# Performance work log

Measured on AMD Instinct MI355X. Metric: run time of the kernel, lower is better.

## Reference

```python
import jax, jax.numpy as jnp
import numpy as np

B, TIN, E, TOUT, NMEL = 32, 512, 576, 400, 80
PRE, ARNN, DRNN, ADIM, NF, KS = 256, 1024, 1024, 128, 32, 31


def setup_inputs() -> dict:
    key = jax.random.key(0)
    ks = jax.random.split(key, 24)
    r = lambda i, sh, s=0.02: jax.random.normal(ks[i], sh, dtype=jnp.float32) * s
    return {
        'memory': jax.random.normal(ks[0], (B, TIN, E), dtype=jnp.float32) * 0.5,
        'decoder_inputs': jax.random.normal(ks[1], (B, TOUT, NMEL), dtype=jnp.float32) * 0.5,
        'prenet_W1': r(2, (PRE, NMEL)),
        'prenet_W2': r(3, (PRE, PRE)),
        'att_Wih': r(4, (4 * ARNN, PRE + E)),
        'att_Whh': r(5, (4 * ARNN, ARNN)),
        'att_bih': r(6, (4 * ARNN,)),
        'att_bhh': r(7, (4 * ARNN,)),
        'qW': r(8, (ADIM, ARNN)),
        'memW': r(9, (ADIM, E)),
        'convW': r(10, (NF, 2, KS)),
        'convb': r(11, (NF,)),
        'locW': r(12, (ADIM, NF)),
        'vW': r(13, (ADIM,)),
        'dec_Wih': r(14, (4 * DRNN, ARNN + E)),
        'dec_Whh': r(15, (4 * DRNN, DRNN)),
        'dec_bih': r(16, (4 * DRNN,)),
        'dec_bhh': r(17, (4 * DRNN,)),
        'projW': r(18, (NMEL, DRNN + E)),
        'projb': r(19, (NMEL,)),
        'gateW': r(20, (1, DRNN + E)),
        'gateb': r(21, (1,)),
        'memory_lengths': jnp.clip(jax.random.randint(ks[22], (B,), 1, TIN + 1), 16, TIN),
    }


def _lstm(x, h, c, Wih, Whh, bih, bhh):
    g = x @ Wih.T + bih + h @ Whh.T + bhh
    i, f, gg, o = jnp.split(g, 4, axis=-1)  # torch LSTMCell gate order i,f,g,o
    c = jax.nn.sigmoid(f) * c + jax.nn.sigmoid(i) * jnp.tanh(gg)
    h = jax.nn.sigmoid(o) * jnp.tanh(c)
    return h, c


def _forward(memory, decoder_inputs, prenet_W1, prenet_W2, att_Wih, att_Whh, att_bih,
             att_bhh, qW, memW, convW, convb, locW, vW, dec_Wih, dec_Whh, dec_bih,
             dec_bhh, projW, projb, gateW, gateb, memory_lengths):
    b, tin, e = memory.shape
    # go frame + teacher forcing inputs -> prenet (dropout off in deterministic eval)
    go = jnp.zeros((b, 1, NMEL), dtype=memory.dtype)
    di = jnp.concatenate([go, decoder_inputs], axis=1)          # [B, T+1, NMEL]
    x = jax.nn.relu(di @ prenet_W1.T)
    x = jax.nn.relu(x @ prenet_W2.T)                            # [B, T+1, PRE]
    xs = jnp.swapaxes(x, 0, 1)[:-1]                             # [T, B, PRE]
    pmem = memory @ memW.T                                      # [B, TIN, ADIM]
    invalid = jnp.arange(tin)[None, :] >= memory_lengths[:, None]
    pad = KS // 2

    init = (jnp.zeros((b, ARNN)), jnp.zeros((b, ARNN)),
            jnp.zeros((b, DRNN)), jnp.zeros((b, DRNN)),
            jnp.zeros((b, tin)), jnp.zeros((b, tin)),
            jnp.zeros((b, e)))

    def step(carry, xt):
        ah, ac, dh, dc, aw, awc, ctx = carry
        ci = jnp.concatenate([xt, ctx], axis=-1)
        ah, ac = _lstm(ci, ah, ac, att_Wih, att_Whh, att_bih, att_bhh)
        ah = ac  # faithful to source: dropout(attention_cell) overwrites hidden (identity in eval)
        wc = jnp.stack([aw, awc], axis=1)                       # [B, 2, TIN]
        loc = jax.lax.conv_general_dilated(
            wc, convW, (1,), [(pad, pad)],
            dimension_numbers=('NCH', 'OIH', 'NCH')) + convb[None, :, None]
        loc = jnp.swapaxes(loc, 1, 2) @ locW.T                  # [B, TIN, ADIM]
        q = (ah @ qW.T)[:, None, :]                             # [B, 1, ADIM]
        en = jnp.tanh(q + pmem + loc) @ vW                      # [B, TIN]
        en = jnp.where(invalid, -jnp.inf, en)
        aw = jax.nn.softmax(en, axis=1)
        ctx = jnp.einsum('bt,bte->be', aw, memory)
        awc = awc + aw
        d_in = jnp.concatenate([ah, ctx], axis=-1)
        dh, dc = _lstm(d_in, dh, dc, dec_Wih, dec_Whh, dec_bih, dec_bhh)
        dhc = jnp.concatenate([dh, ctx], axis=-1)
        mel = dhc @ projW.T + projb                             # [B, NMEL]
        gate = (dhc @ gateW.T + gateb)[:, 0]                    # [B]
        return (ah, ac, dh, dc, aw, awc, ctx), (mel, gate, aw)

    _, (mels, gates, aligns) = jax.lax.scan(step, init, xs)
    mel_out = jnp.swapaxes(jnp.swapaxes(mels, 0, 1), 1, 2)      # [B, NMEL, T]
    gate_out = jnp.swapaxes(gates, 0, 1)                        # [B, T]
    align_out = jnp.swapaxes(aligns, 0, 1)                      # [B, T, TIN]
    return mel_out, gate_out, align_out


def reference(memory, decoder_inputs, prenet_W1, prenet_W2, att_Wih, att_Whh, att_bih,
              att_bhh, qW, memW, convW, convb, locW, vW, dec_Wih, dec_Whh, dec_bih,
              dec_bhh, projW, projb, gateW, gateb, memory_lengths):
    return _forward(memory, decoder_inputs, prenet_W1, prenet_W2, att_Wih, att_Whh,
                    att_bih, att_bhh, qW, memW, convW, convb, locW, vW, dec_Wih,
                    dec_Whh, dec_bih, dec_bhh, projW, projb, gateW, gateb,
                    memory_lengths)
```

## Files before the change

### kernel.cpp

```cpp
#include <hip/hip_runtime.h>
#include <stdint.h>


#define NB  32
#define TI  512
#define ED  576
#define TO  400
#define NM  80
#define PR  256
#define AR  1024
#define DR  1024
#define AD  128
#define NFl 32
#define KSz 31
#define KA  1856
#define KD  2624
#define NKT_A 58
#define NKT_D 82
#define REL_IDX 320
#define MF_OFF  512

#define SCR_CWB 3584
#define SCR_ACC 4608
#define SCR_DCC 4736
#define SCR_SQ  4864
#define LDS_WA_BYTES (NKT_A*512*2)
#define LDS_WD_BYTES (NKT_D*512*2)
#define LDS_SCR_FLOATS 4992
#define LDS_TOTAL (LDS_WA_BYTES + LDS_WD_BYTES + LDS_SCR_FLOATS*4)

typedef __attribute__((ext_vector_type(8))) short bf8_t;
typedef __attribute__((ext_vector_type(4))) float f4_t;
typedef __attribute__((ext_vector_type(2))) float f2_t;
typedef unsigned long long ull;

__device__ __forceinline__ short f2bf(float f){
  union { float f; unsigned u; } v; v.f = f;
  unsigned r = v.u + 0x7fffu + ((v.u >> 16) & 1u);
  return (short)(r >> 16);
}
__device__ __forceinline__ float bf2f(short s){
  union { unsigned u; float f; } v; v.u = ((unsigned)(unsigned short)s) << 16; return v.f;
}
__device__ __forceinline__ float sigm(float x){ return 1.f / (1.f + __expf(-x)); }

__device__ __forceinline__ f4_t MFMA(bf8_t a, bf8_t b, f4_t c){
  return __builtin_amdgcn_mfma_f32_16x16x32_bf16(a, b, c, 0, 0, 0);
}

__device__ __forceinline__ float cld(const float* p){
  return __hip_atomic_load(p, __ATOMIC_RELAXED, __HIP_MEMORY_SCOPE_AGENT);
}
__device__ __forceinline__ void cst(float* p, float v){
  __hip_atomic_store(p, v, __ATOMIC_RELAXED, __HIP_MEMORY_SCOPE_AGENT);
}
__device__ __forceinline__ ull cld8(const void* p){
  return __hip_atomic_load((const ull*)p, __ATOMIC_RELAXED, __HIP_MEMORY_SCOPE_AGENT);
}
__device__ __forceinline__ void cst8(void* p, ull v){
  __hip_atomic_store((ull*)p, v, __ATOMIC_RELAXED, __HIP_MEMORY_SCOPE_AGENT);
}
__device__ __forceinline__ bf8_t cld_bf8(const short* p){
  union { bf8_t v; ull q[2]; } u;
  u.q[0] = cld8(p); u.q[1] = cld8(p + 4);
  return u.v;
}
__device__ __forceinline__ void cst_bf8(short* p, bf8_t v){
  union { bf8_t v; ull q[2]; } u; u.v = v;
  cst8(p, u.q[0]); cst8(p + 4, u.q[1]);
}

__device__ __forceinline__ bf8_t packrow(const float* p){
  f4_t a = *(const f4_t*)p;
  f4_t b = *(const f4_t*)(p + 4);
  bf8_t r;
  r[0]=f2bf(a[0]); r[1]=f2bf(a[1]); r[2]=f2bf(a[2]); r[3]=f2bf(a[3]);
  r[4]=f2bf(b[0]); r[5]=f2bf(b[1]); r[6]=f2bf(b[2]); r[7]=f2bf(b[3]);
  return r;
}
__device__ __forceinline__ bf8_t packrow_coh(const float* p){
  union { ull q; float f[2]; } u0, u1, u2, u3;
  u0.q = cld8(p); u1.q = cld8(p + 2); u2.q = cld8(p + 4); u3.q = cld8(p + 6);
  bf8_t r;
  r[0]=f2bf(u0.f[0]); r[1]=f2bf(u0.f[1]);
  r[2]=f2bf(u1.f[0]); r[3]=f2bf(u1.f[1]);
  r[4]=f2bf(u2.f[0]); r[5]=f2bf(u2.f[1]);
  r[6]=f2bf(u3.f[0]); r[7]=f2bf(u3.f[1]);
  return r;
}

struct Par {
  const float *X2, *PMEM;
  const short *WA, *WD, *WQ, *WLOC, *MEMBT, *PJW;
  const float *BSA, *BSD;
  const float *convW, *convb, *vW;
  const float *projb, *gateb;
  const int *mlen;
  float *AC, *DH, *CTX, *AW, *AWC, *EN, *QP;
  short *ABA, *ABD;
  float *out_mel, *out_gate, *out_align;
  unsigned *FLAGS;
};

__device__ __forceinline__ const float* aptr_att(const Par& p, int rp, int t, int b, int k){
  if (k < PR)      return p.X2 + ((size_t)t*NB + b)*PR + k;
  if (k < PR+ED)   return p.CTX + (size_t)rp*NB*ED + b*ED + (k - PR);
  return p.AC + (size_t)b*AR + (k - PR - ED);
}

__device__ __forceinline__ void loadD(const Par& p, int cpar, int ks, int lane,
                                      bf8_t& a0, bf8_t& a1){
  if (ks >= 32 && ks < 50){
    const int kb = ks*32 + ((lane >> 4) << 3);
    const float* c0 = p.CTX + (size_t)cpar*NB*ED + (size_t)(lane & 15)*ED + (kb - AR);
    const float* c1 = p.CTX + (size_t)cpar*NB*ED + (size_t)(16 + (lane & 15))*ED + (kb - AR);
    a0 = packrow_coh(c0);
    a1 = packrow_coh(c1);
  } else {
    a0 = cld_bf8(p.ABD + ((size_t)(0*NKT_D + ks)*64 + lane)*8);
    a1 = cld_bf8(p.ABD + ((size_t)(1*NKT_D + ks)*64 + lane)*8);
  }
}

__device__ __forceinline__ void gbar(unsigned* flags, unsigned tgt){
  __syncthreads();
  if (threadIdx.x == 0)
    __hip_atomic_store(&flags[blockIdx.x], tgt, __ATOMIC_RELAXED, __HIP_MEMORY_SCOPE_AGENT);
  if (blockIdx.x == 0){
    if (threadIdx.x < 256){
      while (__hip_atomic_load(&flags[threadIdx.x], __ATOMIC_RELAXED, __HIP_MEMORY_SCOPE_AGENT) < tgt) {}
    }
    __syncthreads();
    if (threadIdx.x == 0)
      __hip_atomic_store(&flags[REL_IDX], tgt, __ATOMIC_RELAXED, __HIP_MEMORY_SCOPE_AGENT);
  }
  if (threadIdx.x == 0){
    while (__hip_atomic_load(&flags[REL_IDX], __ATOMIC_RELAXED, __HIP_MEMORY_SCOPE_AGENT) < tgt) {}
  }
  __syncthreads();
}

__device__ __forceinline__ void sibbar(unsigned* mf, int bid, int tid, unsigned tgt){
  __syncthreads();
  if (tid == 0)
    __hip_atomic_store(&mf[bid], tgt, __ATOMIC_RELAXED, __HIP_MEMORY_SCOPE_AGENT);
  const int g = (bid >> 3) << 3;
  if (tid < 8){
    while (__hip_atomic_load(&mf[g + tid], __ATOMIC_RELAXED, __HIP_MEMORY_SCOPE_AGENT) < tgt) {}
  }
  __syncthreads();
}

__device__ __forceinline__ void reduce8(float* scr, f4_t& a0, f4_t& a1, int lane, int wv){
  if (wv > 0){
    float* slot = scr + (size_t)((wv - 1)*64 + lane)*8;
    *(f4_t*)slot       = a0;
    *(f4_t*)(slot + 4) = a1;
  }
  __syncthreads();
  if (wv == 0){
    #pragma unroll
    for (int w = 0; w < 7; ++w){
      const float* s2 = scr + (size_t)(w*64 + lane)*8;
      a0 += *(const f4_t*)s2;
      a1 += *(const f4_t*)(s2 + 4);
    }
  }
  __syncthreads();
}

__device__ __forceinline__ void dec_gates_cell(const Par& p, const short* sWD, float* scr,
                                               float* sDCc, int cpar, int bid,
                                               int lane, int wv, int tid){
  f4_t acc0 = (f4_t){0.f,0.f,0.f,0.f}, acc1 = (f4_t){0.f,0.f,0.f,0.f};
  {
    bf8_t A0[6], A1[6];
    #pragma unroll
    for (int i = 0; i < 6; ++i) loadD(p, cpar, wv + i*8, lane, A0[i], A1[i]);
    #pragma unroll
    for (int i = 0; i < 6; ++i){
      const bf8_t bw = *((const bf8_t*)sWD + (wv + i*8)*64 + lane);
      acc0 = MFMA(A0[i], bw, acc0);
      acc1 = MFMA(A1[i], bw, acc1);
    }
  }
  {
    bf8_t A0[5], A1[5];
    #pragma unroll
    for (int i = 0; i < 5; ++i){
      const int ks = wv + (i + 6)*8;
      if (ks < NKT_D) loadD(p, cpar, ks, lane, A0[i], A1[i]);
    }
    #pragma unroll
    for (int i = 0; i < 5; ++i){
      const int ks = wv + (i + 6)*8;
      if (ks < NKT_D){
        const bf8_t bw = *((const bf8_t*)sWD + ks*64 + lane);
        acc0 = MFMA(A0[i], bw, acc0);
        acc1 = MFMA(A1[i], bw, acc1);
      }
    }
  }
  reduce8(scr, acc0, acc1, lane, wv);
  float* sG = scr;
  if (wv == 0){
    const int col = lane & 15, rb2 = (lane >> 4) << 2;
    const int jp = (col & 3)*1024 + bid*4 + (col >> 2);
    const float bs = p.BSD[jp];
    #pragma unroll
    for (int r = 0; r < 4; ++r){
      sG[(rb2 + r)*16 + col]      = acc0[r] + bs;
      sG[(16 + rb2 + r)*16 + col] = acc1[r] + bs;
    }
  }
  __syncthreads();
  if (tid < 128){
    const int b = tid >> 2, ul = tid & 3;
    const float gi = sG[b*16 + ul*4 + 0];
    const float gf = sG[b*16 + ul*4 + 1];
    const float gg = sG[b*16 + ul*4 + 2];
    const float go = sG[b*16 + ul*4 + 3];
    const float c  = sigm(gf) * sDCc[tid] + sigm(gi) * tanhf(gg);
    sDCc[tid] = c;
    cst(&p.DH[(size_t)b*DR + bid*4 + ul], sigm(go) * tanhf(c));
  }
  __syncthreads();
}

__device__ void dec_proj(const Par& p, int b, int tprev, int tid, float* sIN){
  const float* ctxg = p.CTX + (size_t)(tprev & 1)*NB*ED + b*ED;
  float h0  = cld(&p.DH[(size_t)b*DR + tid]);
  float h1  = cld(&p.DH[(size_t)b*DR + 512 + tid]);
  float cx0 = cld(ctxg + tid);
  float cx1 = (tid < ED - 512) ? cld(ctxg + 512 + tid) : 0.f;
  sIN[tid] = h0; sIN[512 + tid] = h1;
  sIN[1024 + tid] = cx0;
  if (tid < ED - 512) sIN[1536 + tid] = cx1;
  if (tid < 448) sIN[1600 + tid] = 0.f;
  __syncthreads();
  const int lane = tid & 63, wv = tid >> 6;
  for (int o = wv; o < 81; o += 8){
    const short* wr = p.PJW + (size_t)o*2048 + lane*8;
    float s = 0.f;
    #pragma unroll
    for (int j = 0; j < 4; ++j){
      const bf8_t w8 = *(const bf8_t*)(wr + j*512);
      const float* v = sIN + j*512 + lane*8;
      s += v[0]*bf2f(w8[0]) + v[1]*bf2f(w8[1]) + v[2]*bf2f(w8[2]) + v[3]*bf2f(w8[3])
         + v[4]*bf2f(w8[4]) + v[5]*bf2f(w8[5]) + v[6]*bf2f(w8[6]) + v[7]*bf2f(w8[7]);
    }
    #pragma unroll
    for (int d = 32; d > 0; d >>= 1) s += __shfl_down(s, d);
    if (lane == 0){
      if (o < 80) p.out_mel[((size_t)b*NM + o)*TO + tprev] = s + p.projb[o];
      else        p.out_gate[(size_t)b*TO + tprev] = s + p.gateb[0];
    }
  }
  __syncthreads();
}

__global__ __launch_bounds__(512) void k_loop(Par p){
  const int bid = blockIdx.x, tid = threadIdx.x;
  const int lane = tid & 63, wv = tid >> 6;

  extern __shared__ char dsm[];
  short* sWA = (short*)dsm;
  short* sWD = (short*)(dsm + LDS_WA_BYTES);
  float* scr = (float*)(dsm + LDS_WA_BYTES + LDS_WD_BYTES);
  float* sACc = scr + SCR_ACC;
  float* sDCc = scr + SCR_DCC;
  unsigned* mf = p.FLAGS + MF_OFF;

  {
    if (tid < 128){ sACc[tid] = 0.f; sDCc[tid] = 0.f; }
    const bf8_t* gwa = (const bf8_t*)(p.WA + (size_t)bid*NKT_A*512);
    bf8_t* lwa = (bf8_t*)sWA;
    for (int i = tid; i < NKT_A*64; i += 512) lwa[i] = gwa[i];
    const bf8_t* gwd = (const bf8_t*)(p.WD + (size_t)bid*NKT_D*512);
    bf8_t* lwd = (bf8_t*)sWD;
    for (int i = tid; i < NKT_D*64; i += 512) lwd[i] = gwd[i];
    __syncthreads();
  }

  for (int t = 0; t < TO; ++t){
    const int wp = t & 1, rp = wp ^ 1;
    const unsigned base = (unsigned)(t * 3);

    {
      f4_t acc0 = (f4_t){0.f,0.f,0.f,0.f}, acc1 = (f4_t){0.f,0.f,0.f,0.f};
      bf8_t A0[8], A1[8];
      #pragma unroll
      for (int i = 0; i < 8; ++i){
        const int ks = wv + i*8;
        if (ks < NKT_A){
          if (t == 0 || (ks >= 8 && ks < 26)){
            const int kb = ks*32 + ((lane >> 4) << 3);
            const float* p0 = aptr_att(p, rp, t, lane & 15, kb);
            const float* p1 = aptr_att(p, rp, t, 16 + (lane & 15), kb);
            if (kb < PR){ A0[i] = packrow(p0);     A1[i] = packrow(p1);     }
            else        { A0[i] = packrow_coh(p0); A1[i] = packrow_coh(p1); }
          } else {
            A0[i] = cld_bf8(p.ABA + ((size_t)(0*NKT_A + ks)*64 + lane)*8);
            A1[i] = cld_bf8(p.ABA + ((size_t)(1*NKT_A + ks)*64 + lane)*8);
          }
        }
      }
      #pragma unroll
      for (int i = 0; i < 8; ++i){
        const int ks = wv + i*8;
        if (ks < NKT_A){
          const bf8_t bw = *((const bf8_t*)sWA + ks*64 + lane);
          acc0 = MFMA(A0[i], bw, acc0);
          acc1 = MFMA(A1[i], bw, acc1);
        }
      }
      reduce8(scr, acc0, acc1, lane, wv);
      float* sG = scr;
      if (wv == 0){
        const int col = lane & 15, rb2 = (lane >> 4) << 2;
        const int jp = (col & 3)*1024 + bid*4 + (col >> 2);
        const float bs = p.BSA[jp];
        #pragma unroll
        for (int r = 0; r < 4; ++r){
          sG[(rb2 + r)*16 + col]      = acc0[r] + bs;
          sG[(16 + rb2 + r)*16 + col] = acc1[r] + bs;
        }
      }
      __syncthreads();
      if (tid < 128){
        const int b = tid >> 2, ul = tid & 3;
        const float gi = sG[b*16 + ul*4 + 0];
        const float gf = sG[b*16 + ul*4 + 1];
        const float gg = sG[b*16 + ul*4 + 2];
        const float c  = sigm(gf) * sACc[tid] + sigm(gi) * tanhf(gg);
        sACc[tid] = c;
        cst(&p.AC[(size_t)b*AR + bid*4 + ul], c);
      }
      __syncthreads();
      if (t > 0) dec_gates_cell(p, sWD, scr, sDCc, rp, bid, lane, wv, tid);
      const int b = bid >> 3, tc = bid & 7, t0 = tc*64;
      float* sAWI = scr;
      short* sCwB = (short*)(scr + SCR_CWB);
      for (int i = tid; i < 94; i += 512){
        int g = t0 - 15 + i;
        float a = 0.f, w = 0.f;
        if (g >= 0 && g < TI){
          a = cld(&p.AW [(size_t)rp*NB*TI + b*TI + g]);
          w = cld(&p.AWC[(size_t)rp*NB*TI + b*TI + g]);
        }
        sAWI[2*i] = a; sAWI[2*i + 1] = w;
      }
      __syncthreads();
      {
        const int wvu = __builtin_amdgcn_readfirstlane(wv);
        const int f0 = wvu * 4;
        float ac4[4];
        #pragma unroll
        for (int ff = 0; ff < 4; ++ff) ac4[ff] = p.convb[f0 + ff];
        for (int k = 0; k < KSz; ++k){
          f2_t a2 = *(const f2_t*)&sAWI[2*(lane + k)];
          #pragma unroll
          for (int ff = 0; ff < 4; ++ff){
            ac4[ff] += a2[0] * p.convW[((f0+ff)*2 + 0)*KSz + k]
                     + a2[1] * p.convW[((f0+ff)*2 + 1)*KSz + k];
          }
        }
        #pragma unroll
        for (int ff = 0; ff < 4; ++ff) sCwB[lane*32 + f0 + ff] = f2bf(ac4[ff]);
      }
    }
    gbar(p.FLAGS, base + 1);

    {
      if (bid < 32){
        const int nt = bid >> 2, kc = bid & 3;
        const int kt = kc*8 + wv;
        const int kb = kt*32 + ((lane >> 4) << 3);
        bf8_t a0 = packrow_coh(p.AC + (size_t)(lane & 15)*AR + kb);
        bf8_t a1 = packrow_coh(p.AC + (size_t)(16 + (lane & 15))*AR + kb);
        const bf8_t bw = *(const bf8_t*)(p.WQ + ((size_t)(nt*32 + kt)*64 + lane)*8);
        f4_t q0 = (f4_t){0.f,0.f,0.f,0.f}, q1 = (f4_t){0.f,0.f,0.f,0.f};
        q0 = MFMA(a0, bw, q0);
        q1 = MFMA(a1, bw, q1);
        reduce8(scr, q0, q1, lane, wv);
        if (wv == 0){
          const int col = lane & 15, rb2 = (lane >> 4) << 2;
          float* qp = p.QP + (size_t)kc*NB*AD;
          #pragma unroll
          for (int r = 0; r < 4; ++r){
            cst(&qp[(rb2 + r)*AD + nt*16 + col],      q0[r]);
            cst(&qp[(16 + rb2 + r)*AD + nt*16 + col], q1[r]);
          }
        }
      }
      if (bid >= 224 && t > 0) dec_proj(p, bid - 224, t - 1, tid, scr);
    }
    gbar(p.FLAGS, base + 2);

    {
      float* sQ = scr + SCR_SQ;
      if (tid < 128){
        const int b = bid >> 3;
        sQ[tid] = cld(&p.QP[(size_t)b*AD + tid])
                + cld(&p.QP[(size_t)NB*AD + b*AD + tid])
                + cld(&p.QP[(size_t)2*NB*AD + b*AD + tid])
                + cld(&p.QP[(size_t)3*NB*AD + b*AD + tid]);
      }
      if (wv == 0 && bid < 208){
        const int r = lane & 15, koff = (lane >> 4) << 3;
        if (bid < 80){
          if (t < TO - 1){
            const int m = bid / 40, idx = bid % 40;
            const int ks = (idx < 8) ? idx : idx + 18;
            const int row = m*16 + r;
            const int k = ks*32 + koff;
            bf8_t v = (k < PR)
              ? packrow(p.X2 + ((size_t)(t+1)*NB + row)*PR + k)
              : packrow_coh(p.AC + (size_t)row*AR + (k - PR - ED));
            cst_bf8(p.ABA + ((size_t)(m*NKT_A + ks)*64 + lane)*8, v);
          }
        } else {
          const int j2 = bid - 80;
          const int m = j2 / 64, idx = j2 % 64;
          const int ks = (idx < 32) ? idx : idx + 18;
          const int row = m*16 + r;
          const int k = ks*32 + koff;
          bf8_t v = (k < AR)
            ? packrow_coh(p.AC + (size_t)row*AR + k)
            : packrow_coh(p.DH + (size_t)row*DR + (k - AR - ED));
          cst_bf8(p.ABD + ((size_t)(m*NKT_D + ks)*64 + lane)*8, v);
        }
      }
      __syncthreads();
      const int b = bid >> 3, tc = bid & 7, t0 = tc*64;
      short* sCwB = (short*)(scr + SCR_CWB);
      float* eP = scr;
      const int g = lane >> 4, li = lane & 15;
      const int d2 = wv*16 + li;
      const float vw = p.vW[d2];
      const float qd = sQ[d2];
      const bf8_t bfr = *(const bf8_t*)(p.WLOC + (size_t)(wv*64 + lane)*8);
      #pragma unroll
      for (int mt = 0; mt < 4; ++mt){
        const bf8_t afr = *(const bf8_t*)(sCwB + (mt*16 + li)*32 + (g << 3));
        f4_t c = (f4_t){0.f,0.f,0.f,0.f};
        c = MFMA(afr, bfr, c);
        #pragma unroll
        for (int r = 0; r < 4; ++r){
          const int tg = t0 + mt*16 + g*4 + r;
          const float val = c[r] + p.PMEM[((size_t)b*TI + tg)*AD + d2];
          float v = vw * tanhf(qd + val);
          v += __shfl_xor(v, 1);
          v += __shfl_xor(v, 2);
          v += __shfl_xor(v, 4);
          v += __shfl_xor(v, 8);
          if (li == 0) eP[wv*64 + mt*16 + g*4 + r] = v;
        }
      }
      __syncthreads();
      if (tid < 64){
        float e = eP[tid];
        #pragma unroll
        for (int w2 = 1; w2 < 8; ++w2) e += eP[w2*64 + tid];
        const int tg = t0 + tid;
        cst(&p.EN[b*TI + tg], (tg < p.mlen[b]) ? e : -1e30f);
      }
    }
    sibbar(mf, bid, tid, (unsigned)(t + 1));

    {
      const int b = bid >> 3, ec = bid & 7;
      float* red = scr;
      float* sp  = scr + 64;
      const float e = cld(&p.EN[b*TI + tid]);
      float m = e;
      #pragma unroll
      for (int d = 32; d > 0; d >>= 1) m = fmaxf(m, __shfl_xor(m, d));
      if (lane == 0) red[wv] = m;
      __syncthreads();
      const float M = fmaxf(fmaxf(fmaxf(red[0], red[1]), fmaxf(red[2], red[3])),
                            fmaxf(fmaxf(red[4], red[5]), fmaxf(red[6], red[7])));
      const float x = __expf(e - M);
      float z = x;
      #pragma unroll
      for (int d = 32; d > 0; d >>= 1) z += __shfl_xor(z, d);
      __syncthreads();
      if (lane == 0) red[wv] = z;
      __syncthreads();
      const float Z = red[0]+red[1]+red[2]+red[3]+red[4]+red[5]+red[6]+red[7];
      const float pv = x / Z;
      sp[tid] = pv;
      __syncthreads();
      if (ec == 0){
        cst(&p.AW [(size_t)wp*NB*TI + b*TI + tid], pv);
        cst(&p.AWC[(size_t)wp*NB*TI + b*TI + tid],
            cld(&p.AWC[(size_t)rp*NB*TI + b*TI + tid]) + pv);
        p.out_align[((size_t)b*TO + t)*TI + tid] = pv;
      }
      #pragma unroll
      for (int ii = 0; ii < 9; ++ii){
        const int e2 = ec*72 + wv*9 + ii;
        const short* row = p.MEMBT + ((size_t)b*ED + e2)*TI;
        const bf8_t w8 = *(const bf8_t*)(row + lane*8);
        const float* v = sp + lane*8;
        float a2 = v[0]*bf2f(w8[0]) + v[1]*bf2f(w8[1]) + v[2]*bf2f(w8[2]) + v[3]*bf2f(w8[3])
                 + v[4]*bf2f(w8[4]) + v[5]*bf2f(w8[5]) + v[6]*bf2f(w8[6]) + v[7]*bf2f(w8[7]);
        #pragma unroll
        for (int d = 32; d > 0; d >>= 1) a2 += __shfl_down(a2, d);
        if (lane == 0)
          cst(&p.CTX[(size_t)wp*NB*ED + b*ED + e2], a2);
      }
    }
    gbar(p.FLAGS, base + 3);
  }

  dec_gates_cell(p, sWD, scr, sDCc, (TO - 1) & 1, bid, lane, wv, tid);
  gbar(p.FLAGS, (unsigned)(TO*3 + 1));
  if (bid >= 224) dec_proj(p, bid - 224, TO - 1, tid, scr);
}

__global__ __launch_bounds__(256) void k_init(float* z, int nz,
                                              float* bsa, const float* a1, const float* a2,
                                              float* bsd, const float* d1, const float* d2){
  const int idx = blockIdx.x*256 + threadIdx.x, st = gridDim.x*256;
  const int NG = 4096;
  for (int i = idx; i < nz; i += st) z[i] = 0.f;
  for (int i = idx; i < NG; i += st){ bsa[i] = a1[i] + a2[i]; bsd[i] = d1[i] + d2[i]; }
}

__global__ __launch_bounds__(256) void k_prenet1(const float* di, const float* W1, float* X1){
  const int t = blockIdx.x, tid = threadIdx.x;
  __shared__ float sdi[NB*NM];
  for (int i = tid; i < NB*NM; i += 256){
    const int b = i / NM, k = i - b*NM;
    sdi[i] = (t == 0) ? 0.f : di[((size_t)b*TO + (t-1))*NM + k];
  }
  __syncthreads();
  float acc[NB];
  #pragma unroll
  for (int b = 0; b < NB; ++b) acc[b] = 0.f;
  const int j = tid;
  for (int k = 0; k < NM; ++k){
    const float w = W1[j*NM + k];
    #pragma unroll
    for (int b = 0; b < NB; ++b) acc[b] += sdi[b*NM + k] * w;
  }
  for (int b = 0; b < NB; ++b)
    X1[((size_t)t*NB + b)*PR + j] = fmaxf(acc[b], 0.f);
}

__global__ __launch_bounds__(256) void k_prenet2(const float* X1, const float* W2, float* X2){
  const int t = blockIdx.x, tid = threadIdx.x;
  __shared__ float sx[NB*PR];
  for (int i = tid; i < NB*PR; i += 256) sx[i] = X1[(size_t)t*NB*PR + i];
  __syncthreads();
  float acc[NB];
  #pragma unroll
  for (int b = 0; b < NB; ++b) acc[b] = 0.f;
  const int j = tid;
  for (int k = 0; k < PR; ++k){
    const float w = W2[j*PR + k];
    #pragma unroll
    for (int b = 0; b < NB; ++b) acc[b] += sx[b*PR + k] * w;
  }
  for (int b = 0; b < NB; ++b)
    X2[((size_t)t*NB + b)*PR + j] = fmaxf(acc[b], 0.f);
}

__global__ __launch_bounds__(256) void k_pmem(const float* mem, const float* memW, float* pm){
  const int b = blockIdx.x >> 3, tc = blockIdx.x & 7, tid = threadIdx.x;
  __shared__ float sW[64*AD];
  __shared__ float sM[64*65];
  const int tl = tid >> 2, dq = tid & 3;
  float acc[32];
  #pragma unroll
  for (int i = 0; i < 32; ++i) acc[i] = 0.f;
  for (int kc = 0; kc < 9; ++kc){
    __syncthreads();
    for (int i = tid; i < 64*AD; i += 256){
      const int d = i >> 6, kl = i & 63;
      sW[kl*AD + ((d + kl) & 127)] = memW[(size_t)d*ED + kc*64 + kl];
    }
    for (int i = tid; i < 64*64; i += 256){
      const int tt = i >> 6, kl = i & 63;
      sM[tt*65 + kl] = mem[((size_t)b*TI + tc*64 + tt)*ED + kc*64 + kl];
    }
    __syncthreads();
    for (int kl = 0; kl < 64; ++kl){
      const float mv = sM[tl*65 + kl];
      #pragma unroll
      for (int d2 = 0; d2 < 32; ++d2)
        acc[d2] += mv * sW[kl*AD + ((dq*32 + d2 + kl) & 127)];
    }
  }
  for (int d2 = 0; d2 < 32; ++d2)
    pm[((size_t)b*TI + tc*64 + tl)*AD + dq*32 + d2] = acc[d2];
}

__global__ __launch_bounds__(256) void k_membt(const float* mem, short* mt){
  const int b = blockIdx.x / 36, ec = blockIdx.x % 36;
  __shared__ float sT[64*17];
  for (int tc = 0; tc < 8; ++tc){
    __syncthreads();
    for (int i = threadIdx.x; i < 64*16; i += 256){
      const int tt = i >> 4, e = i & 15;
      sT[tt*17 + e] = mem[((size_t)b*TI + tc*64 + tt)*ED + ec*16 + e];
    }
    __syncthreads();
    for (int i = threadIdx.x; i < 16*64; i += 256){
      const int e = i >> 6, tt = i & 63;
      mt[((size_t)b*ED + ec*16 + e)*TI + tc*64 + tt] = f2bf(sT[tt*17 + e]);
    }
  }
}

__global__ __launch_bounds__(64) void k_swz_gate(const float* Wih, const float* Whh,
                                                 short* dst, int split, int nkt){
  const int bidx = blockIdx.x;
  const int nt = bidx / nkt, kt = bidx - nt*nkt;
  const int lane = threadIdx.x;
  const int nl = lane & 15;
  const int jp = (nl & 3)*1024 + nt*4 + (nl >> 2);
  const int k0 = kt*32 + ((lane >> 4) << 3);
  bf8_t v;
  #pragma unroll
  for (int jj = 0; jj < 8; ++jj){
    const int k = k0 + jj;
    const float f = (k < split) ? Wih[(size_t)jp*split + k]
                                : Whh[(size_t)jp*1024 + (k - split)];
    v[jj] = f2bf(f);
  }
  *(bf8_t*)(dst + (size_t)bidx*512 + lane*8) = v;
}

__global__ __launch_bounds__(64) void k_swz_q(const float* qW, short* dst){
  const int bidx = blockIdx.x;
  const int nt = bidx >> 5, kt = bidx & 31;
  const int lane = threadIdx.x;
  const int d = nt*16 + (lane & 15);
  const int k0 = kt*32 + ((lane >> 4) << 3);
  bf8_t v;
  #pragma unroll
  for (int jj = 0; jj < 8; ++jj) v[jj] = f2bf(qW[(size_t)d*AR + k0 + jj]);
  *(bf8_t*)(dst + (size_t)bidx*512 + lane*8) = v;
}

__global__ __launch_bounds__(64) void k_swz_loc(const float* locW, short* dst){
  const int nt = blockIdx.x;
  const int lane = threadIdx.x;
  const int d = nt*16 + (lane & 15);
  const int f0 = (lane >> 4) << 3;
  bf8_t v;
  #pragma unroll
  for (int jj = 0; jj < 8; ++jj) v[jj] = f2bf(locW[d*NFl + f0 + jj]);
  *(bf8_t*)(dst + (size_t)(nt*64 + lane)*8) = v;
}

__global__ __launch_bounds__(256) void k_swz_proj(const float* projW, const float* gateW,
                                                  short* dst){
  const int o = blockIdx.x;
  const float* src = (o < 80) ? (projW + (size_t)o*1600) : gateW;
  for (int k = threadIdx.x; k < 2048; k += 256)
    dst[(size_t)o*2048 + k] = (k < 1600) ? f2bf(src[k]) : (short)0;
}

extern "C" void kernel_launch(void* const* d_in, const int* in_sizes, int n_in,
                              void* d_out, int out_size, void* d_ws, size_t ws_size,
                              hipStream_t stream){
  const float* mem    = (const float*)d_in[0];
  const float* dec_in = (const float*)d_in[1];
  const float* pW1    = (const float*)d_in[2];
  const float* pW2    = (const float*)d_in[3];
  const float* aWih   = (const float*)d_in[4];
  const float* aWhh   = (const float*)d_in[5];
  const float* aBih   = (const float*)d_in[6];
  const float* aBhh   = (const float*)d_in[7];
  const float* qW     = (const float*)d_in[8];
  const float* memW   = (const float*)d_in[9];
  const float* convW  = (const float*)d_in[10];
  const float* convb  = (const float*)d_in[11];
  const float* locW   = (const float*)d_in[12];
  const float* vW     = (const float*)d_in[13];
  const float* dWih   = (const float*)d_in[14];
  const float* dWhh   = (const float*)d_in[15];
  const float* dBih   = (const float*)d_in[16];
  const float* dBhh   = (const float*)d_in[17];
  const float* projW  = (const float*)d_in[18];
  const float* projb  = (const float*)d_in[19];
  const float* gateW  = (const float*)d_in[20];
  const float* gateb  = (const float*)d_in[21];
  const int*   mlen   = (const int*)d_in[22];
  (void)in_sizes; (void)n_in; (void)out_size; (void)ws_size;

  char* basep = (char*)d_ws;
  size_t off = 0;
  auto carve = [&](size_t bytes) -> char* {
    char* r = basep + off;
    off = (off + bytes + 255) & ~(size_t)255;
    return r;
  };
  const int NG = 4096;
  short* WA    = (short*)carve((size_t)NG*KA*2);
  short* WD    = (short*)carve((size_t)NG*KD*2);
  short* WQ    = (short*)carve((size_t)AD*AR*2);
  short* WLOC  = (short*)carve((size_t)AD*NFl*2);
  short* MEMBT = (short*)carve((size_t)NB*TI*ED*2);
  short* PJW   = (short*)carve((size_t)81*2048*2);
  float* X1    = (float*)carve((size_t)TO*NB*PR*4);
  float* X2    = (float*)carve((size_t)TO*NB*PR*4);
  float* PMEM  = (float*)carve((size_t)NB*TI*AD*4);
  float* BSA   = (float*)carve((size_t)NG*4);
  float* BSD   = (float*)carve((size_t)NG*4);
  short* ABA   = (short*)carve((size_t)2*NKT_A*512*2);
  short* ABD   = (short*)carve((size_t)2*NKT_D*512*2);
  float* AC    = (float*)carve((size_t)NB*AR*4);
  float* DH    = (float*)carve((size_t)NB*DR*4);
  float* CTX   = (float*)carve((size_t)2*NB*ED*4);
  float* AW    = (float*)carve((size_t)2*NB*TI*4);
  float* AWC   = (float*)carve((size_t)2*NB*TI*4);
  float* EN    = (float*)carve((size_t)NB*TI*4);
  float* QP    = (float*)carve((size_t)4*NB*AD*4);
  unsigned* FLAGS = (unsigned*)carve(4096);
  const int nz = (int)((((char*)FLAGS + 4096) - (char*)AC) / 4);

  float* out_mel   = (float*)d_out;
  float* out_gate  = out_mel + (size_t)NB*NM*TO;
  float* out_align = out_gate + (size_t)NB*TO;

  k_init   <<<dim3(512), dim3(256), 0, stream>>>(AC, nz, BSA, aBih, aBhh, BSD, dBih, dBhh);
  k_prenet1<<<dim3(TO),  dim3(256), 0, stream>>>(dec_in, pW1, X1);
  k_prenet2<<<dim3(TO),  dim3(256), 0, stream>>>(X1, pW2, X2);
  k_pmem   <<<dim3(256), dim3(256), 0, stream>>>(mem, memW, PMEM);
  k_membt  <<<dim3(NB*36), dim3(256), 0, stream>>>(mem, MEMBT);
  k_swz_gate<<<dim3(256*NKT_A), dim3(64), 0, stream>>>(aWih, aWhh, WA, 832, NKT_A);
  k_swz_gate<<<dim3(256*NKT_D), dim3(64), 0, stream>>>(dWih, dWhh, WD, 1600, NKT_D);
  k_swz_q  <<<dim3(256), dim3(64), 0, stream>>>(qW, WQ);
  k_swz_loc<<<dim3(8),   dim3(64), 0, stream>>>(locW, WLOC);
  k_swz_proj<<<dim3(81), dim3(256), 0, stream>>>(projW, gateW, PJW);

  Par p;
  p.X2 = X2; p.PMEM = PMEM;
  p.WA = WA; p.WD = WD; p.WQ = WQ; p.WLOC = WLOC; p.MEMBT = MEMBT; p.PJW = PJW;
  p.BSA = BSA; p.BSD = BSD;
  p.convW = convW; p.convb = convb; p.vW = vW;
  p.projb = projb; p.gateb = gateb;
  p.mlen = mlen;
  p.AC = AC; p.DH = DH; p.CTX = CTX;
  p.AW = AW; p.AWC = AWC; p.EN = EN; p.QP = QP;
  p.ABA = ABA; p.ABD = ABD;
  p.out_mel = out_mel; p.out_gate = out_gate; p.out_align = out_align;
  p.FLAGS = FLAGS;

  (void)hipFuncSetAttribute((const void*)k_loop,
                            hipFuncAttributeMaxDynamicSharedMemorySize, LDS_TOTAL);
  k_loop<<<dim3(256), dim3(512), LDS_TOTAL, stream>>>(p);
}
```

Measured before the change: 32.43 ms.

## Restructure persistent decoder step to two grid barriers with overlapped gate GEMMs

Reorganizes the per-timestep schedule of the persistent decoder kernel from three grid barriers to two. The attention-LSTM and decoder-LSTM gate matmul parts that depend only on prior hidden states are issued before the first barrier, with the context-dependent parts finished afterwards. It drops the staged bf16 A-buffers (ABA/ABD) and the precomputed query buffer in favour of direct coherent loads from AC/DH/CTX, and pre-swizzles the prenet output into MFMA fragments in a new setup kernel. LDS reduction and conv scratch layouts are padded to avoid bank conflicts, and the final projection is spread across all blocks. The trade-off is more redundant global-memory reads per block and more complex dependency ordering inside each step.

```diff
diff --git a/kernel.cpp b/kernel.cpp
--- a/kernel.cpp
+++ b/kernel.cpp
@@ -20,18 +20,17 @@
 #define REL_IDX 320
 #define MF_OFF  512
 
-#define SCR_CWB 3584
-#define SCR_ACC 4608
-#define SCR_DCC 4736
-#define SCR_SQ  4864
+#define SCR_CWB 3640
+#define SCR_ACC 4664
+#define SCR_DCC 4792
+#define SCR_SQ  4920
 #define LDS_WA_BYTES (NKT_A*512*2)
 #define LDS_WD_BYTES (NKT_D*512*2)
-#define LDS_SCR_FLOATS 4992
+#define LDS_SCR_FLOATS 5048
 #define LDS_TOTAL (LDS_WA_BYTES + LDS_WD_BYTES + LDS_SCR_FLOATS*4)
 
 typedef __attribute__((ext_vector_type(8))) short bf8_t;
 typedef __attribute__((ext_vector_type(4))) float f4_t;
-typedef __attribute__((ext_vector_type(2))) float f2_t;
 typedef unsigned long long ull;
 
 __device__ __forceinline__ short f2bf(float f){
@@ -57,27 +56,7 @@
 __device__ __forceinline__ ull cld8(const void* p){
   return __hip_atomic_load((const ull*)p, __ATOMIC_RELAXED, __HIP_MEMORY_SCOPE_AGENT);
 }
-__device__ __forceinline__ void cst8(void* p, ull v){
-  __hip_atomic_store((ull*)p, v, __ATOMIC_RELAXED, __HIP_MEMORY_SCOPE_AGENT);
-}
-__device__ __forceinline__ bf8_t cld_bf8(const short* p){
-  union { bf8_t v; ull q[2]; } u;
-  u.q[0] = cld8(p); u.q[1] = cld8(p + 4);
-  return u.v;
-}
-__device__ __forceinline__ void cst_bf8(short* p, bf8_t v){
-  union { bf8_t v; ull q[2]; } u; u.v = v;
-  cst8(p, u.q[0]); cst8(p + 4, u.q[1]);
-}
-
-__device__ __forceinline__ bf8_t packrow(const float* p){
-  f4_t a = *(const f4_t*)p;
-  f4_t b = *(const f4_t*)(p + 4);
-  bf8_t r;
-  r[0]=f2bf(a[0]); r[1]=f2bf(a[1]); r[2]=f2bf(a[2]); r[3]=f2bf(a[3]);
-  r[4]=f2bf(b[0]); r[5]=f2bf(b[1]); r[6]=f2bf(b[2]); r[7]=f2bf(b[3]);
-  return r;
-}
+
 __device__ __forceinline__ bf8_t packrow_coh(const float* p){
   union { ull q; float f[2]; } u0, u1, u2, u3;
   u0.q = cld8(p); u1.q = cld8(p + 2); u2.q = cld8(p + 4); u3.q = cld8(p + 6);
@@ -91,36 +70,38 @@
 
 struct Par {
   const float *X2, *PMEM;
-  const short *WA, *WD, *WQ, *WLOC, *MEMBT, *PJW;
+  const short *WA, *WD, *WLOC, *MEMBT, *PJW, *X2F, *QWP;
   const float *BSA, *BSD;
   const float *convW, *convb, *vW;
   const float *projb, *gateb;
   const int *mlen;
-  float *AC, *DH, *CTX, *AW, *AWC, *EN, *QP;
-  short *ABA, *ABD;
+  float *AC, *DH, *CTX, *AW, *AWC, *EN;
   float *out_mel, *out_gate, *out_align;
   unsigned *FLAGS;
 };
 
-__device__ __forceinline__ const float* aptr_att(const Par& p, int rp, int t, int b, int k){
-  if (k < PR)      return p.X2 + ((size_t)t*NB + b)*PR + k;
-  if (k < PR+ED)   return p.CTX + (size_t)rp*NB*ED + b*ED + (k - PR);
-  return p.AC + (size_t)b*AR + (k - PR - ED);
-}
-
-__device__ __forceinline__ void loadD(const Par& p, int cpar, int ks, int lane,
-                                      bf8_t& a0, bf8_t& a1){
-  if (ks >= 32 && ks < 50){
-    const int kb = ks*32 + ((lane >> 4) << 3);
-    const float* c0 = p.CTX + (size_t)cpar*NB*ED + (size_t)(lane & 15)*ED + (kb - AR);
-    const float* c1 = p.CTX + (size_t)cpar*NB*ED + (size_t)(16 + (lane & 15))*ED + (kb - AR);
-    a0 = packrow_coh(c0);
-    a1 = packrow_coh(c1);
-  } else {
-    a0 = cld_bf8(p.ABD + ((size_t)(0*NKT_D + ks)*64 + lane)*8);
-    a1 = cld_bf8(p.ABD + ((size_t)(1*NKT_D + ks)*64 + lane)*8);
-  }
-}
+__device__ __forceinline__ void ldAH(const Par& p, int ks, int lane, bf8_t& a0, bf8_t& a1){
+  const int kb = ks*32 + ((lane >> 4) << 3) - (PR + ED);
+  a0 = packrow_coh(p.AC + (size_t)(lane & 15)*AR + kb);
+  a1 = packrow_coh(p.AC + (size_t)(16 + (lane & 15))*AR + kb);
+}
+__device__ __forceinline__ void ldDC(const Par& p, int ks, int lane, bf8_t& a0, bf8_t& a1){
+  const int kb = ks*32 + ((lane >> 4) << 3);
+  a0 = packrow_coh(p.AC + (size_t)(lane & 15)*AR + kb);
+  a1 = packrow_coh(p.AC + (size_t)(16 + (lane & 15))*AR + kb);
+}
+__device__ __forceinline__ void ldDHf(const Par& p, int ks, int lane, bf8_t& a0, bf8_t& a1){
+  const int kb = ks*32 + ((lane >> 4) << 3) - (AR + ED);
+  a0 = packrow_coh(p.DH + (size_t)(lane & 15)*DR + kb);
+  a1 = packrow_coh(p.DH + (size_t)(16 + (lane & 15))*DR + kb);
+}
+__device__ __forceinline__ void ldCT(const Par& p, int cpar, int ks, int sub, int lane,
+                                     bf8_t& a0, bf8_t& a1){
+  const int kb = ks*32 + ((lane >> 4) << 3) - sub;
+  a0 = packrow_coh(p.CTX + (size_t)cpar*NB*ED + (size_t)(lane & 15)*ED + kb);
+  a1 = packrow_coh(p.CTX + (size_t)cpar*NB*ED + (size_t)(16 + (lane & 15))*ED + kb);
+}
+#define WFR(s, ks) (*((const bf8_t*)(s) + (ks)*64 + lane))
 
 __device__ __forceinline__ void gbar(unsigned* flags, unsigned tgt){
   __syncthreads();
@@ -153,102 +134,42 @@
 
 __device__ __forceinline__ void reduce8(float* scr, f4_t& a0, f4_t& a1, int lane, int wv){
   if (wv > 0){
-    float* slot = scr + (size_t)((wv - 1)*64 + lane)*8;
-    *(f4_t*)slot       = a0;
-    *(f4_t*)(slot + 4) = a1;
+    float* base = scr + (size_t)(wv - 1)*520;
+    #pragma unroll
+    for (int e = 0; e < 4; ++e) base[e*65 + lane] = a0[e];
+    #pragma unroll
+    for (int e = 0; e < 4; ++e) base[(4 + e)*65 + lane] = a1[e];
   }
   __syncthreads();
   if (wv == 0){
     #pragma unroll
     for (int w = 0; w < 7; ++w){
-      const float* s2 = scr + (size_t)(w*64 + lane)*8;
-      a0 += *(const f4_t*)s2;
-      a1 += *(const f4_t*)(s2 + 4);
-    }
-  }
-  __syncthreads();
-}
-
-__device__ __forceinline__ void dec_gates_cell(const Par& p, const short* sWD, float* scr,
-                                               float* sDCc, int cpar, int bid,
-                                               int lane, int wv, int tid){
-  f4_t acc0 = (f4_t){0.f,0.f,0.f,0.f}, acc1 = (f4_t){0.f,0.f,0.f,0.f};
-  {
-    bf8_t A0[6], A1[6];
-    #pragma unroll
-    for (int i = 0; i < 6; ++i) loadD(p, cpar, wv + i*8, lane, A0[i], A1[i]);
-    #pragma unroll
-    for (int i = 0; i < 6; ++i){
-      const bf8_t bw = *((const bf8_t*)sWD + (wv + i*8)*64 + lane);
-      acc0 = MFMA(A0[i], bw, acc0);
-      acc1 = MFMA(A1[i], bw, acc1);
-    }
-  }
-  {
-    bf8_t A0[5], A1[5];
-    #pragma unroll
-    for (int i = 0; i < 5; ++i){
-      const int ks = wv + (i + 6)*8;
-      if (ks < NKT_D) loadD(p, cpar, ks, lane, A0[i], A1[i]);
-    }
-    #pragma unroll
-    for (int i = 0; i < 5; ++i){
-      const int ks = wv + (i + 6)*8;
-      if (ks < NKT_D){
-        const bf8_t bw = *((const bf8_t*)sWD + ks*64 + lane);
-        acc0 = MFMA(A0[i], bw, acc0);
-        acc1 = MFMA(A1[i], bw, acc1);
-      }
-    }
-  }
-  reduce8(scr, acc0, acc1, lane, wv);
-  float* sG = scr;
-  if (wv == 0){
-    const int col = lane & 15, rb2 = (lane >> 4) << 2;
-    const int jp = (col & 3)*1024 + bid*4 + (col >> 2);
-    const float bs = p.BSD[jp];
-    #pragma unroll
-    for (int r = 0; r < 4; ++r){
-      sG[(rb2 + r)*16 + col]      = acc0[r] + bs;
-      sG[(16 + rb2 + r)*16 + col] = acc1[r] + bs;
-    }
-  }
-  __syncthreads();
-  if (tid < 128){
-    const int b = tid >> 2, ul = tid & 3;
-    const float gi = sG[b*16 + ul*4 + 0];
-    const float gf = sG[b*16 + ul*4 + 1];
-    const float gg = sG[b*16 + ul*4 + 2];
-    const float go = sG[b*16 + ul*4 + 3];
-    const float c  = sigm(gf) * sDCc[tid] + sigm(gi) * tanhf(gg);
-    sDCc[tid] = c;
-    cst(&p.DH[(size_t)b*DR + bid*4 + ul], sigm(go) * tanhf(c));
-  }
-  __syncthreads();
-}
-
-__device__ void dec_proj(const Par& p, int b, int tprev, int tid, float* sIN){
+      const float* base = scr + (size_t)w*520;
+      #pragma unroll
+      for (int e = 0; e < 4; ++e) a0[e] += base[e*65 + lane];
+      #pragma unroll
+      for (int e = 0; e < 4; ++e) a1[e] += base[(4 + e)*65 + lane];
+    }
+  }
+  __syncthreads();
+}
+
+__device__ void proj_dist(const Par& p, int b, int r8, int tprev,
+                          int tid, int lane, int wv, float* sIN2){
+  sIN2[tid]        = cld(&p.DH[(size_t)b*DR + tid]);
+  sIN2[512 + tid]  = cld(&p.DH[(size_t)b*DR + 512 + tid]);
   const float* ctxg = p.CTX + (size_t)(tprev & 1)*NB*ED + b*ED;
-  float h0  = cld(&p.DH[(size_t)b*DR + tid]);
-  float h1  = cld(&p.DH[(size_t)b*DR + 512 + tid]);
-  float cx0 = cld(ctxg + tid);
-  float cx1 = (tid < ED - 512) ? cld(ctxg + 512 + tid) : 0.f;
-  sIN[tid] = h0; sIN[512 + tid] = h1;
-  sIN[1024 + tid] = cx0;
-  if (tid < ED - 512) sIN[1536 + tid] = cx1;
-  if (tid < 448) sIN[1600 + tid] = 0.f;
-  __syncthreads();
-  const int lane = tid & 63, wv = tid >> 6;
-  for (int o = wv; o < 81; o += 8){
-    const short* wr = p.PJW + (size_t)o*2048 + lane*8;
+  sIN2[1024 + tid] = cld(ctxg + tid);
+  if (tid < 64) sIN2[1536 + tid] = cld(ctxg + 512 + tid);
+  __syncthreads();
+  const int no = (r8 == 7) ? 11 : 10, o0 = r8*10;
+  for (int oi = wv; oi < no; oi += 8){
+    const int o = o0 + oi;
+    const short* wr = p.PJW + (size_t)o*2048;
     float s = 0.f;
     #pragma unroll
-    for (int j = 0; j < 4; ++j){
-      const bf8_t w8 = *(const bf8_t*)(wr + j*512);
-      const float* v = sIN + j*512 + lane*8;
-      s += v[0]*bf2f(w8[0]) + v[1]*bf2f(w8[1]) + v[2]*bf2f(w8[2]) + v[3]*bf2f(w8[3])
-         + v[4]*bf2f(w8[4]) + v[5]*bf2f(w8[5]) + v[6]*bf2f(w8[6]) + v[7]*bf2f(w8[7]);
-    }
+    for (int i2 = 0; i2 < 25; ++i2)
+      s += sIN2[lane + 64*i2] * bf2f(wr[lane + 64*i2]);
     #pragma unroll
     for (int d = 32; d > 0; d >>= 1) s += __shfl_down(s, d);
     if (lane == 0){
@@ -284,37 +205,99 @@
 
   for (int t = 0; t < TO; ++t){
     const int wp = t & 1, rp = wp ^ 1;
-    const unsigned base = (unsigned)(t * 3);
+    const unsigned base = (unsigned)(t * 2);
+
+    f4_t aA0 = (f4_t){0.f,0.f,0.f,0.f}, aA1 = (f4_t){0.f,0.f,0.f,0.f};
+    f4_t aD0 = (f4_t){0.f,0.f,0.f,0.f}, aD1 = (f4_t){0.f,0.f,0.f,0.f};
 
     {
-      f4_t acc0 = (f4_t){0.f,0.f,0.f,0.f}, acc1 = (f4_t){0.f,0.f,0.f,0.f};
-      bf8_t A0[8], A1[8];
-      #pragma unroll
-      for (int i = 0; i < 8; ++i){
-        const int ks = wv + i*8;
-        if (ks < NKT_A){
-          if (t == 0 || (ks >= 8 && ks < 26)){
-            const int kb = ks*32 + ((lane >> 4) << 3);
-            const float* p0 = aptr_att(p, rp, t, lane & 15, kb);
-            const float* p1 = aptr_att(p, rp, t, 16 + (lane & 15), kb);
-            if (kb < PR){ A0[i] = packrow(p0);     A1[i] = packrow(p1);     }
-            else        { A0[i] = packrow_coh(p0); A1[i] = packrow_coh(p1); }
-          } else {
-            A0[i] = cld_bf8(p.ABA + ((size_t)(0*NKT_A + ks)*64 + lane)*8);
-            A1[i] = cld_bf8(p.ABA + ((size_t)(1*NKT_A + ks)*64 + lane)*8);
-          }
+      {
+        const bf8_t* xf = (const bf8_t*)p.X2F + ((size_t)t*8 + wv)*128;
+        const bf8_t x0 = xf[lane];
+        const bf8_t x1 = xf[64 + lane];
+        const int ab = (wv < 2) ? (wv + 32) : (wv + 24);
+        bf8_t h00,h01,h10,h11,h20,h21,h30,h31;
+        ldAH(p, ab +  0, lane, h00, h01);
+        ldAH(p, ab +  8, lane, h10, h11);
+        ldAH(p, ab + 16, lane, h20, h21);
+        ldAH(p, ab + 24, lane, h30, h31);
+        aA0 = MFMA(x0, WFR(sWA, wv), aA0);
+        aA1 = MFMA(x1, WFR(sWA, wv), aA1);
+        aA0 = MFMA(h00, WFR(sWA, ab +  0), aA0);
+        aA1 = MFMA(h01, WFR(sWA, ab +  0), aA1);
+        aA0 = MFMA(h10, WFR(sWA, ab +  8), aA0);
+        aA1 = MFMA(h11, WFR(sWA, ab +  8), aA1);
+        aA0 = MFMA(h20, WFR(sWA, ab + 16), aA0);
+        aA1 = MFMA(h21, WFR(sWA, ab + 16), aA1);
+        aA0 = MFMA(h30, WFR(sWA, ab + 24), aA0);
+        aA1 = MFMA(h31, WFR(sWA, ab + 24), aA1);
+      }
+      {
+        bf8_t c00,c01,c10,c11,c20,c21,c30,c31;
+        ldDC(p, wv +  0, lane, c00, c01);
+        ldDC(p, wv +  8, lane, c10, c11);
+        ldDC(p, wv + 16, lane, c20, c21);
+        ldDC(p, wv + 24, lane, c30, c31);
+        aD0 = MFMA(c00, WFR(sWD, wv +  0), aD0);
+        aD1 = MFMA(c01, WFR(sWD, wv +  0), aD1);
+        aD0 = MFMA(c10, WFR(sWD, wv +  8), aD0);
+        aD1 = MFMA(c11, WFR(sWD, wv +  8), aD1);
+        aD0 = MFMA(c20, WFR(sWD, wv + 16), aD0);
+        aD1 = MFMA(c21, WFR(sWD, wv + 16), aD1);
+        aD0 = MFMA(c30, WFR(sWD, wv + 24), aD0);
+        aD1 = MFMA(c31, WFR(sWD, wv + 24), aD1);
+      }
+      {
+        const int db = (wv < 2) ? (wv + 56) : (wv + 48);
+        bf8_t h00,h01,h10,h11,h20,h21,h30,h31;
+        ldDHf(p, db +  0, lane, h00, h01);
+        ldDHf(p, db +  8, lane, h10, h11);
+        ldDHf(p, db + 16, lane, h20, h21);
+        ldDHf(p, db + 24, lane, h30, h31);
+        aD0 = MFMA(h00, WFR(sWD, db +  0), aD0);
+        aD1 = MFMA(h01, WFR(sWD, db +  0), aD1);
+        aD0 = MFMA(h10, WFR(sWD, db +  8), aD0);
+        aD1 = MFMA(h11, WFR(sWD, db +  8), aD1);
+        aD0 = MFMA(h20, WFR(sWD, db + 16), aD0);
+        aD1 = MFMA(h21, WFR(sWD, db + 16), aD1);
+        aD0 = MFMA(h30, WFR(sWD, db + 24), aD0);
+        aD1 = MFMA(h31, WFR(sWD, db + 24), aD1);
+      }
+    }
+    gbar(p.FLAGS, base + 1);
+
+    {
+      const int bb = bid >> 3, tc = bid & 7, t0 = tc*64;
+      float cva = 0.f, cvw = 0.f;
+      if (tid < 94){
+        const int g = t0 - 15 + tid;
+        if (g >= 0 && g < TI){
+          cva = cld(&p.AW [(size_t)rp*NB*TI + bb*TI + g]);
+          cvw = cld(&p.AWC[(size_t)rp*NB*TI + bb*TI + g]);
         }
       }
-      #pragma unroll
-      for (int i = 0; i < 8; ++i){
-        const int ks = wv + i*8;
-        if (ks < NKT_A){
-          const bf8_t bw = *((const bf8_t*)sWA + ks*64 + lane);
-          acc0 = MFMA(A0[i], bw, acc0);
-          acc1 = MFMA(A1[i], bw, acc1);
+      {
+        bf8_t c00,c01,c10,c11,c20,c21;
+        const bool c_ok = (wv < 2);
+        ldCT(p, rp, wv +  8, PR, lane, c00, c01);
+        ldCT(p, rp, wv + 16, PR, lane, c10, c11);
+        if (c_ok) ldCT(p, rp, wv + 24, PR, lane, c20, c21);
+        aA0 = MFMA(c00, WFR(sWA, wv +  8), aA0);
+        aA1 = MFMA(c01, WFR(sWA, wv +  8), aA1);
+        aA0 = MFMA(c10, WFR(sWA, wv + 16), aA0);
+        aA1 = MFMA(c11, WFR(sWA, wv + 16), aA1);
+        if (c_ok){
+          aA0 = MFMA(c20, WFR(sWA, wv + 24), aA0);
+          aA1 = MFMA(c21, WFR(sWA, wv + 24), aA1);
         }
       }
-      reduce8(scr, acc0, acc1, lane, wv);
+      bf8_t d00,d01,d10,d11,d20,d21;
+      const bool dc_ok = (wv < 2);
+      ldCT(p, rp, wv + 32, AR, lane, d00, d01);
+      ldCT(p, rp, wv + 40, AR, lane, d10, d11);
+      if (dc_ok) ldCT(p, rp, wv + 48, AR, lane, d20, d21);
+
+      reduce8(scr, aA0, aA1, lane, wv);
       float* sG = scr;
       if (wv == 0){
         const int col = lane & 15, rb2 = (lane >> 4) << 2;
@@ -322,8 +305,8 @@
         const float bs = p.BSA[jp];
         #pragma unroll
         for (int r = 0; r < 4; ++r){
-          sG[(rb2 + r)*16 + col]      = acc0[r] + bs;
-          sG[(16 + rb2 + r)*16 + col] = acc1[r] + bs;
+          sG[(rb2 + r)*16 + col]      = aA0[r] + bs;
+          sG[(16 + rb2 + r)*16 + col] = aA1[r] + bs;
         }
       }
       __syncthreads();
@@ -337,19 +320,40 @@
         cst(&p.AC[(size_t)b*AR + bid*4 + ul], c);
       }
       __syncthreads();
-      if (t > 0) dec_gates_cell(p, sWD, scr, sDCc, rp, bid, lane, wv, tid);
-      const int b = bid >> 3, tc = bid & 7, t0 = tc*64;
+      aD0 = MFMA(d00, WFR(sWD, wv + 32), aD0);
+      aD1 = MFMA(d01, WFR(sWD, wv + 32), aD1);
+      aD0 = MFMA(d10, WFR(sWD, wv + 40), aD0);
+      aD1 = MFMA(d11, WFR(sWD, wv + 40), aD1);
+      if (dc_ok){
+        aD0 = MFMA(d20, WFR(sWD, wv + 48), aD0);
+        aD1 = MFMA(d21, WFR(sWD, wv + 48), aD1);
+      }
+      reduce8(scr, aD0, aD1, lane, wv);
+      if (wv == 0){
+        const int col = lane & 15, rb2 = (lane >> 4) << 2;
+        const int jp = (col & 3)*1024 + bid*4 + (col >> 2);
+        const float bs = p.BSD[jp];
+        #pragma unroll
+        for (int r = 0; r < 4; ++r){
+          sG[(rb2 + r)*16 + col]      = aD0[r] + bs;
+          sG[(16 + rb2 + r)*16 + col] = aD1[r] + bs;
+        }
+      }
+      __syncthreads();
+      if (t > 0 && tid < 128){
+        const int b = tid >> 2, ul = tid & 3;
+        const float gi = sG[b*16 + ul*4 + 0];
+        const float gf = sG[b*16 + ul*4 + 1];
+        const float gg = sG[b*16 + ul*4 + 2];
+        const float go = sG[b*16 + ul*4 + 3];
+        const float c  = sigm(gf) * sDCc[tid] + sigm(gi) * tanhf(gg);
+        sDCc[tid] = c;
+        cst(&p.DH[(size_t)b*DR + bid*4 + ul], sigm(go) * tanhf(c));
+      }
+      __syncthreads();
       float* sAWI = scr;
       short* sCwB = (short*)(scr + SCR_CWB);
-      for (int i = tid; i < 94; i += 512){
-        int g = t0 - 15 + i;
-        float a = 0.f, w = 0.f;
-        if (g >= 0 && g < TI){
-          a = cld(&p.AW [(size_t)rp*NB*TI + b*TI + g]);
-          w = cld(&p.AWC[(size_t)rp*NB*TI + b*TI + g]);
-        }
-        sAWI[2*i] = a; sAWI[2*i + 1] = w;
-      }
+      if (tid < 94){ sAWI[3*tid] = cva; sAWI[3*tid + 1] = cvw; }
       __syncthreads();
       {
         const int wvu = __builtin_amdgcn_readfirstlane(wv);
@@ -358,83 +362,47 @@
         #pragma unroll
         for (int ff = 0; ff < 4; ++ff) ac4[ff] = p.convb[f0 + ff];
         for (int k = 0; k < KSz; ++k){
-          f2_t a2 = *(const f2_t*)&sAWI[2*(lane + k)];
+          const float av  = sAWI[3*(lane + k)];
+          const float wcv = sAWI[3*(lane + k) + 1];
           #pragma unroll
           for (int ff = 0; ff < 4; ++ff){
-            ac4[ff] += a2[0] * p.convW[((f0+ff)*2 + 0)*KSz + k]
-                     + a2[1] * p.convW[((f0+ff)*2 + 1)*KSz + k];
+            ac4[ff] += av  * p.convW[((f0+ff)*2 + 0)*KSz + k]
+                     + wcv * p.convW[((f0+ff)*2 + 1)*KSz + k];
           }
         }
         #pragma unroll
         for (int ff = 0; ff < 4; ++ff) sCwB[lane*32 + f0 + ff] = f2bf(ac4[ff]);
       }
     }
-    gbar(p.FLAGS, base + 1);
+    gbar(p.FLAGS, base + 2);
 
     {
-      if (bid < 32){
-        const int nt = bid >> 2, kc = bid & 3;
-        const int kt = kc*8 + wv;
-        const int kb = kt*32 + ((lane >> 4) << 3);
-        bf8_t a0 = packrow_coh(p.AC + (size_t)(lane & 15)*AR + kb);
-        bf8_t a1 = packrow_coh(p.AC + (size_t)(16 + (lane & 15))*AR + kb);
-        const bf8_t bw = *(const bf8_t*)(p.WQ + ((size_t)(nt*32 + kt)*64 + lane)*8);
-        f4_t q0 = (f4_t){0.f,0.f,0.f,0.f}, q1 = (f4_t){0.f,0.f,0.f,0.f};
-        q0 = MFMA(a0, bw, q0);
-        q1 = MFMA(a1, bw, q1);
-        reduce8(scr, q0, q1, lane, wv);
-        if (wv == 0){
-          const int col = lane & 15, rb2 = (lane >> 4) << 2;
-          float* qp = p.QP + (size_t)kc*NB*AD;
-          #pragma unroll
-          for (int r = 0; r < 4; ++r){
-            cst(&qp[(rb2 + r)*AD + nt*16 + col],      q0[r]);
-            cst(&qp[(16 + rb2 + r)*AD + nt*16 + col], q1[r]);
-          }
+      const int b = bid >> 3, r8 = bid & 7, t0 = r8*64;
+      float* sACrow = scr;
+      float* sIN2   = scr + 1024;
+      float* eP     = scr + 2624;
+      float* sQ     = scr + SCR_SQ;
+      sACrow[tid]       = cld(&p.AC[(size_t)b*AR + tid]);
+      sACrow[512 + tid] = cld(&p.AC[(size_t)b*AR + 512 + tid]);
+      __syncthreads();
+      {
+        const int d = wv*16 + (lane & 15), qq = lane >> 4;
+        float acc = 0.f;
+        const short* qwp = p.QWP + (size_t)qq*32*1024 + d*8;
+        #pragma unroll
+        for (int i = 0; i < 32; ++i){
+          const bf8_t w8 = *(const bf8_t*)(qwp + i*1024);
+          const float* av = sACrow + qq*256 + i*8;
+          acc += av[0]*bf2f(w8[0]) + av[1]*bf2f(w8[1]) + av[2]*bf2f(w8[2]) + av[3]*bf2f(w8[3])
+               + av[4]*bf2f(w8[4]) + av[5]*bf2f(w8[5]) + av[6]*bf2f(w8[6]) + av[7]*bf2f(w8[7]);
         }
-      }
-      if (bid >= 224 && t > 0) dec_proj(p, bid - 224, t - 1, tid, scr);
-    }
-    gbar(p.FLAGS, base + 2);
-
-    {
-      float* sQ = scr + SCR_SQ;
-      if (tid < 128){
-        const int b = bid >> 3;
-        sQ[tid] = cld(&p.QP[(size_t)b*AD + tid])
-                + cld(&p.QP[(size_t)NB*AD + b*AD + tid])
-                + cld(&p.QP[(size_t)2*NB*AD + b*AD + tid])
-                + cld(&p.QP[(size_t)3*NB*AD + b*AD + tid]);
-      }
-      if (wv == 0 && bid < 208){
-        const int r = lane & 15, koff = (lane >> 4) << 3;
-        if (bid < 80){
-          if (t < TO - 1){
-            const int m = bid / 40, idx = bid % 40;
-            const int ks = (idx < 8) ? idx : idx + 18;
-            const int row = m*16 + r;
-            const int k = ks*32 + koff;
-            bf8_t v = (k < PR)
-              ? packrow(p.X2 + ((size_t)(t+1)*NB + row)*PR + k)
-              : packrow_coh(p.AC + (size_t)row*AR + (k - PR - ED));
-            cst_bf8(p.ABA + ((size_t)(m*NKT_A + ks)*64 + lane)*8, v);
-          }
-        } else {
-          const int j2 = bid - 80;
-          const int m = j2 / 64, idx = j2 % 64;
-          const int ks = (idx < 32) ? idx : idx + 18;
-          const int row = m*16 + r;
-          const int k = ks*32 + koff;
-          bf8_t v = (k < AR)
-            ? packrow_coh(p.AC + (size_t)row*AR + k)
-            : packrow_coh(p.DH + (size_t)row*DR + (k - AR - ED));
-          cst_bf8(p.ABD + ((size_t)(m*NKT_D + ks)*64 + lane)*8, v);
-        }
-      }
-      __syncthreads();
-      const int b = bid >> 3, tc = bid & 7, t0 = tc*64;
+        acc += __shfl_down(acc, 32);
+        acc += __shfl_down(acc, 16);
+        if (lane < 16) sQ[wv*16 + lane] = acc;
+      }
+      __syncthreads();
+      if (t > 0) proj_dist(p, b, r8, t - 1, tid, lane, wv, sIN2);
       short* sCwB = (short*)(scr + SCR_CWB);
-      float* eP = scr;
       const int g = lane >> 4, li = lane & 15;
       const int d2 = wv*16 + li;
       const float vw = p.vW[d2];
@@ -470,8 +438,8 @@
 
     {
       const int b = bid >> 3, ec = bid & 7;
-      float* red = scr;
-      float* sp  = scr + 64;
+      float* spS = scr;
+      float* red = scr + 576;
       const float e = cld(&p.EN[b*TI + tid]);
       float m = e;
       #pragma unroll
@@ -489,34 +457,107 @@
       __syncthreads();
       const float Z = red[0]+red[1]+red[2]+red[3]+red[4]+red[5]+red[6]+red[7];
       const float pv = x / Z;
-      sp[tid] = pv;
-      __syncthreads();
+      spS[(tid & 7)*72 + (tid >> 3)] = pv;
       if (ec == 0){
         cst(&p.AW [(size_t)wp*NB*TI + b*TI + tid], pv);
         cst(&p.AWC[(size_t)wp*NB*TI + b*TI + tid],
             cld(&p.AWC[(size_t)rp*NB*TI + b*TI + tid]) + pv);
         p.out_align[((size_t)b*TO + t)*TI + tid] = pv;
       }
+      __syncthreads();
       #pragma unroll
       for (int ii = 0; ii < 9; ++ii){
         const int e2 = ec*72 + wv*9 + ii;
         const short* row = p.MEMBT + ((size_t)b*ED + e2)*TI;
         const bf8_t w8 = *(const bf8_t*)(row + lane*8);
-        const float* v = sp + lane*8;
-        float a2 = v[0]*bf2f(w8[0]) + v[1]*bf2f(w8[1]) + v[2]*bf2f(w8[2]) + v[3]*bf2f(w8[3])
-                 + v[4]*bf2f(w8[4]) + v[5]*bf2f(w8[5]) + v[6]*bf2f(w8[6]) + v[7]*bf2f(w8[7]);
+        float a2 = spS[0*72+lane]*bf2f(w8[0]) + spS[1*72+lane]*bf2f(w8[1])
+                 + spS[2*72+lane]*bf2f(w8[2]) + spS[3*72+lane]*bf2f(w8[3])
+                 + spS[4*72+lane]*bf2f(w8[4]) + spS[5*72+lane]*bf2f(w8[5])
+                 + spS[6*72+lane]*bf2f(w8[6]) + spS[7*72+lane]*bf2f(w8[7]);
         #pragma unroll
         for (int d = 32; d > 0; d >>= 1) a2 += __shfl_down(a2, d);
         if (lane == 0)
           cst(&p.CTX[(size_t)wp*NB*ED + b*ED + e2], a2);
       }
     }
-    gbar(p.FLAGS, base + 3);
-  }
-
-  dec_gates_cell(p, sWD, scr, sDCc, (TO - 1) & 1, bid, lane, wv, tid);
-  gbar(p.FLAGS, (unsigned)(TO*3 + 1));
-  if (bid >= 224) dec_proj(p, bid - 224, TO - 1, tid, scr);
+  }
+
+  gbar(p.FLAGS, (unsigned)(2*TO + 1));
+  {
+    const int cpar = (TO - 1) & 1;
+    f4_t d0v = (f4_t){0.f,0.f,0.f,0.f}, d1v = (f4_t){0.f,0.f,0.f,0.f};
+    {
+      bf8_t c00,c01,c10,c11,c20,c21,c30,c31;
+      ldDC(p, wv +  0, lane, c00, c01);
+      ldDC(p, wv +  8, lane, c10, c11);
+      ldDC(p, wv + 16, lane, c20, c21);
+      ldDC(p, wv + 24, lane, c30, c31);
+      d0v = MFMA(c00, WFR(sWD, wv +  0), d0v);
+      d1v = MFMA(c01, WFR(sWD, wv +  0), d1v);
+      d0v = MFMA(c10, WFR(sWD, wv +  8), d0v);
+      d1v = MFMA(c11, WFR(sWD, wv +  8), d1v);
+      d0v = MFMA(c20, WFR(sWD, wv + 16), d0v);
+      d1v = MFMA(c21, WFR(sWD, wv + 16), d1v);
+      d0v = MFMA(c30, WFR(sWD, wv + 24), d0v);
+      d1v = MFMA(c31, WFR(sWD, wv + 24), d1v);
+    }
+    {
+      const int db = (wv < 2) ? (wv + 56) : (wv + 48);
+      bf8_t h00,h01,h10,h11,h20,h21,h30,h31;
+      ldDHf(p, db +  0, lane, h00, h01);
+      ldDHf(p, db +  8, lane, h10, h11);
+      ldDHf(p, db + 16, lane, h20, h21);
+      ldDHf(p, db + 24, lane, h30, h31);
+      d0v = MFMA(h00, WFR(sWD, db +  0), d0v);
+      d1v = MFMA(h01, WFR(sWD, db +  0), d1v);
+      d0v = MFMA(h10, WFR(sWD, db +  8), d0v);
+      d1v = MFMA(h11, WFR(sWD, db +  8), d1v);
+      d0v = MFMA(h20, WFR(sWD, db + 16), d0v);
+      d1v = MFMA(h21, WFR(sWD, db + 16), d1v);
+      d0v = MFMA(h30, WFR(sWD, db + 24), d0v);
+      d1v = MFMA(h31, WFR(sWD, db + 24), d1v);
+    }
+    {
+      bf8_t e00,e01,e10,e11,e20,e21;
+      const bool c_ok = (wv < 2);
+      ldCT(p, cpar, wv + 32, AR, lane, e00, e01);
+      ldCT(p, cpar, wv + 40, AR, lane, e10, e11);
+      if (c_ok) ldCT(p, cpar, wv + 48, AR, lane, e20, e21);
+      d0v = MFMA(e00, WFR(sWD, wv + 32), d0v);
+      d1v = MFMA(e01, WFR(sWD, wv + 32), d1v);
+      d0v = MFMA(e10, WFR(sWD, wv + 40), d0v);
+      d1v = MFMA(e11, WFR(sWD, wv + 40), d1v);
+      if (c_ok){
+        d0v = MFMA(e20, WFR(sWD, wv + 48), d0v);
+        d1v = MFMA(e21, WFR(sWD, wv + 48), d1v);
+      }
+    }
+    reduce8(scr, d0v, d1v, lane, wv);
+    float* sG = scr;
+    if (wv == 0){
+      const int col = lane & 15, rb2 = (lane >> 4) << 2;
+      const int jp = (col & 3)*1024 + bid*4 + (col >> 2);
+      const float bs = p.BSD[jp];
+      #pragma unroll
+      for (int r = 0; r < 4; ++r){
+        sG[(rb2 + r)*16 + col]      = d0v[r] + bs;
+        sG[(16 + rb2 + r)*16 + col] = d1v[r] + bs;
+      }
+    }
+    __syncthreads();
+    if (tid < 128){
+      const int b = tid >> 2, ul = tid & 3;
+      const float gi = sG[b*16 + ul*4 + 0];
+      const float gf = sG[b*16 + ul*4 + 1];
+      const float gg = sG[b*16 + ul*4 + 2];
+      const float go = sG[b*16 + ul*4 + 3];
+      const float c  = sigm(gf) * sDCc[tid] + sigm(gi) * tanhf(gg);
+      sDCc[tid] = c;
+      cst(&p.DH[(size_t)b*DR + bid*4 + ul], sigm(go) * tanhf(c));
+    }
+  }
+  gbar(p.FLAGS, (unsigned)(2*TO + 2));
+  proj_dist(p, bid >> 3, bid & 7, TO - 1, tid, lane, wv, scr + 1024);
 }
 
 __global__ __launch_bounds__(256) void k_init(float* z, int nz,
@@ -565,6 +606,29 @@
   }
   for (int b = 0; b < NB; ++b)
     X2[((size_t)t*NB + b)*PR + j] = fmaxf(acc[b], 0.f);
+}
+
+__global__ __launch_bounds__(64) void k_x2f(const float* X2, short* xf){
+  const int t = blockIdx.x, lane = threadIdx.x;
+  for (int ks = 0; ks < 8; ++ks){
+    for (int m = 0; m < 2; ++m){
+      const int row = m*16 + (lane & 15);
+      const int k0 = ks*32 + ((lane >> 4) << 3);
+      bf8_t v;
+      #pragma unroll
+      for (int j = 0; j < 8; ++j)
+        v[j] = f2bf(X2[((size_t)t*NB + row)*PR + k0 + j]);
+      *(bf8_t*)(xf + (((size_t)t*8 + ks)*2 + m)*512 + lane*8) = v;
+    }
+  }
+}
+
+__global__ __launch_bounds__(128) void k_swz_qt(const float* qW, short* dst){
+  const int kb = blockIdx.x;
+  const int d  = threadIdx.x;
+  #pragma unroll
+  for (int j = 0; j < 8; ++j)
+    dst[(size_t)kb*1024 + d*8 + j] = f2bf(qW[(size_t)d*AR + kb*8 + j]);
 }
 
 __global__ __launch_bounds__(256) void k_pmem(const float* mem, const float* memW, float* pm){
@@ -630,18 +694,6 @@
                                 : Whh[(size_t)jp*1024 + (k - split)];
     v[jj] = f2bf(f);
   }
-  *(bf8_t*)(dst + (size_t)bidx*512 + lane*8) = v;
-}
-
-__global__ __launch_bounds__(64) void k_swz_q(const float* qW, short* dst){
-  const int bidx = blockIdx.x;
-  const int nt = bidx >> 5, kt = bidx & 31;
-  const int lane = threadIdx.x;
-  const int d = nt*16 + (lane & 15);
-  const int k0 = kt*32 + ((lane >> 4) << 3);
-  bf8_t v;
-  #pragma unroll
-  for (int jj = 0; jj < 8; ++jj) v[jj] = f2bf(qW[(size_t)d*AR + k0 + jj]);
   *(bf8_t*)(dst + (size_t)bidx*512 + lane*8) = v;
 }
 
@@ -702,24 +754,22 @@
   const int NG = 4096;
   short* WA    = (short*)carve((size_t)NG*KA*2);
   short* WD    = (short*)carve((size_t)NG*KD*2);
-  short* WQ    = (short*)carve((size_t)AD*AR*2);
+  short* QWP   = (short*)carve((size_t)AD*AR*2);
   short* WLOC  = (short*)carve((size_t)AD*NFl*2);
   short* MEMBT = (short*)carve((size_t)NB*TI*ED*2);
   short* PJW   = (short*)carve((size_t)81*2048*2);
+  short* X2F   = (short*)carve((size_t)TO*16*512*2);
   float* X1    = (float*)carve((size_t)TO*NB*PR*4);
   float* X2    = (float*)carve((size_t)TO*NB*PR*4);
   float* PMEM  = (float*)carve((size_t)NB*TI*AD*4);
   float* BSA   = (float*)carve((size_t)NG*4);
   float* BSD   = (float*)carve((size_t)NG*4);
-  short* ABA   = (short*)carve((size_t)2*NKT_A*512*2);
-  short* ABD   = (short*)carve((size_t)2*NKT_D*512*2);
   float* AC    = (float*)carve((size_t)NB*AR*4);
   float* DH    = (float*)carve((size_t)NB*DR*4);
   float* CTX   = (float*)carve((size_t)2*NB*ED*4);
   float* AW    = (float*)carve((size_t)2*NB*TI*4);
   float* AWC   = (float*)carve((size_t)2*NB*TI*4);
   float* EN    = (float*)carve((size_t)NB*TI*4);
-  float* QP    = (float*)carve((size_t)4*NB*AD*4);
   unsigned* FLAGS = (unsigned*)carve(4096);
   const int nz = (int)((((char*)FLAGS + 4096) - (char*)AC) / 4);
 
@@ -730,24 +780,25 @@
   k_init   <<<dim3(512), dim3(256), 0, stream>>>(AC, nz, BSA, aBih, aBhh, BSD, dBih, dBhh);
   k_prenet1<<<dim3(TO),  dim3(256), 0, stream>>>(dec_in, pW1, X1);
   k_prenet2<<<dim3(TO),  dim3(256), 0, stream>>>(X1, pW2, X2);
+  k_x2f    <<<dim3(TO),  dim3(64),  0, stream>>>(X2, X2F);
   k_pmem   <<<dim3(256), dim3(256), 0, stream>>>(mem, memW, PMEM);
   k_membt  <<<dim3(NB*36), dim3(256), 0, stream>>>(mem, MEMBT);
   k_swz_gate<<<dim3(256*NKT_A), dim3(64), 0, stream>>>(aWih, aWhh, WA, 832, NKT_A);
   k_swz_gate<<<dim3(256*NKT_D), dim3(64), 0, stream>>>(dWih, dWhh, WD, 1600, NKT_D);
-  k_swz_q  <<<dim3(256), dim3(64), 0, stream>>>(qW, WQ);
+  k_swz_qt <<<dim3(128), dim3(128), 0, stream>>>(qW, QWP);
   k_swz_loc<<<dim3(8),   dim3(64), 0, stream>>>(locW, WLOC);
   k_swz_proj<<<dim3(81), dim3(256), 0, stream>>>(projW, gateW, PJW);
 
   Par p;
   p.X2 = X2; p.PMEM = PMEM;
-  p.WA = WA; p.WD = WD; p.WQ = WQ; p.WLOC = WLOC; p.MEMBT = MEMBT; p.PJW = PJW;
+  p.WA = WA; p.WD = WD; p.WLOC = WLOC; p.MEMBT = MEMBT; p.PJW = PJW;
+  p.X2F = X2F; p.QWP = QWP;
   p.BSA = BSA; p.BSD = BSD;
   p.convW = convW; p.convb = convb; p.vW = vW;
   p.projb = projb; p.gateb = gateb;
   p.mlen = mlen;
   p.AC = AC; p.DH = DH; p.CTX = CTX;
-  p.AW = AW; p.AWC = AWC; p.EN = EN; p.QP = QP;
-  p.ABA = ABA; p.ABD = ABD;
+  p.AW = AW; p.AWC = AWC; p.EN = EN;
   p.out_mel = out_mel; p.out_gate = out_gate; p.out_align = out_align;
   p.FLAGS = FLAGS;
 
```

Result: slower. 41.89 ms (+29.2%).
